# Kernel optimization log

Measured on AMD Instinct MI355X. Metric: run time of the kernel, lower is better.

The kernel has to match this reference:

```python
import jax, jax.numpy as jnp
import numpy as np

N = 100000
E = 1600000

def _gcn_layer(x, row, col, W, b):
    # gather neighbor feats then scatter-add into destination rows
    agg = jax.ops.segment_sum(x[col], row, num_segments=N)  # [N, d]
    deg = jax.ops.segment_sum(jnp.ones((row.shape[0],), x.dtype), row, num_segments=N)
    deg = jnp.clip(deg, 1.0, None)[:, None]  # [N, 1]
    return (agg / deg + x) @ W + b

def setup_inputs() -> dict:
    key = jax.random.key(0)
    ks = jax.random.split(key, 6)
    x = jax.random.normal(ks[0], (N, 64), dtype=jnp.float32)
    edge_index = jax.random.randint(ks[1], (2, E), 0, N, dtype=jnp.int64)
    W1 = jax.random.normal(ks[2], (64, 128), dtype=jnp.float32) * 0.1
    b1 = jax.random.normal(ks[3], (128,), dtype=jnp.float32) * 0.1
    W2 = jax.random.normal(ks[4], (128, 64), dtype=jnp.float32) * 0.1
    b2 = jax.random.normal(ks[5], (64,), dtype=jnp.float32) * 0.1
    return {"x": x, "edge_index": edge_index, "W1": W1, "b1": b1, "W2": W2, "b2": b2}

def reference(x, edge_index, W1, b1, W2, b2):
    row, col = edge_index[0], edge_index[1]
    h = jax.nn.relu(_gcn_layer(x, row, col, W1, b1))
    h = _gcn_layer(h, row, col, W2, b2)
    return h
```

## Files before the change

kernel.cpp:

```cpp
#include <hip/hip_runtime.h>
#include <stdint.h>

#define WS_ALIGN(x) (((x) + 255) & ~(size_t)255)
#define RPB 256
#define CAPB 4608
#define NBMAX 512

typedef __attribute__((ext_vector_type(8))) unsigned short ushort8_t;
typedef __attribute__((ext_vector_type(8))) short short8_t;
typedef __attribute__((ext_vector_type(4))) float float4_t;

static __device__ __forceinline__ unsigned short f2bf(float f) {
    unsigned u = __float_as_uint(f);
    unsigned r = (u + 0x7FFFu + ((u >> 16) & 1u)) >> 16;
    return (unsigned short)r;
}
static __device__ __forceinline__ float bf2f(unsigned short s) {
    return __uint_as_float(((unsigned)s) << 16);
}

__global__ __launch_bounds__(256) void prep_kernel(
    const float4* __restrict__ x, ushort4* __restrict__ xb, int n4,
    const float* __restrict__ W1, const float* __restrict__ W2,
    unsigned short* __restrict__ W1t, unsigned short* __restrict__ W2t,
    int* __restrict__ gCursor, int* __restrict__ gTotal, int nb) {
    int i = blockIdx.x * 256 + threadIdx.x;
    if (i < 8192) {
        int k = i >> 7, col = i & 127;
        W1t[col * 64 + k] = f2bf(W1[i]);
    } else if (i < 16384) {
        int j = i - 8192;
        int k = j >> 6, col = j & 63;
        W2t[col * 128 + k] = f2bf(W2[j]);
    }
    int c = i - 16384;
    if (c >= 0 && c < nb) gCursor[c] = c * CAPB;
    if (c == nb) *gTotal = 0;
    int j = i - (16384 + nb + 64);
    if (j >= 0 && j < n4 + 16) {
        ushort4 o = make_ushort4(0, 0, 0, 0);
        if (j < n4) {
            float4 f = x[j];
            o.x = f2bf(f.x); o.y = f2bf(f.y); o.z = f2bf(f.z); o.w = f2bf(f.w);
        }
        xb[j] = o;
    }
}

__global__ __launch_bounds__(256) void bucket_kernel(
    const void* __restrict__ eidx, int E,
    int nb, int* __restrict__ gCursor, unsigned* __restrict__ staging) {
    __shared__ int cnt[NBMAX];
    __shared__ int base[NBMAX];
    __shared__ int sOr;
    int t = threadIdx.x;
    for (int i = t; i < nb; i += 256) cnt[i] = 0;
    if (t == 0) sOr = 0;
    __syncthreads();

    int hv = 0;
    const int* p32 = (const int*)eidx;
    for (int i = t; i < 2048 && i < E; i += 256) hv |= p32[2 * i + 1];
    if (hv) atomicOr(&sOr, 1);
    __syncthreads();
    bool is64 = (sOr == 0);

    int e0 = (blockIdx.x * 256 + t) * 8;
    int m = E - e0; if (m > 8) m = 8; if (m < 0) m = 0;
    int r[8], bk[8], slot[8];
    for (int j = 0; j < m; ++j) {
        r[j] = is64 ? (int)((const long long*)eidx)[e0 + j]
                    : ((const int*)eidx)[e0 + j];
        bk[j] = r[j] >> 8;
        slot[j] = atomicAdd(&cnt[bk[j]], 1);
    }
    __syncthreads();
    for (int i = t; i < nb; i += 256)
        base[i] = cnt[i] ? atomicAdd(&gCursor[i], cnt[i]) : 0;
    __syncthreads();
    for (int j = 0; j < m; ++j) {
        int c = is64 ? (int)((const long long*)eidx)[E + e0 + j]
                     : ((const int*)eidx)[E + e0 + j];
        int dst = base[bk[j]] + slot[j];
        if (dst < (bk[j] + 1) * CAPB)
            staging[dst] = ((unsigned)(r[j] & (RPB - 1)) << 17) | (unsigned)c;
    }
}

__global__ __launch_bounds__(512) void ell_kernel(
    const unsigned* __restrict__ staging, const int* __restrict__ gCursor,
    int* __restrict__ csr, int2* __restrict__ meta,
    int* __restrict__ gTotal, int N) {
    __shared__ unsigned sd[CAPB];
    __shared__ int lcnt[RPB], scan[RPB], lcnt2[RPB];
    __shared__ int bucketBase;
    int b = blockIdx.x, t = threadIdx.x;
    if (t < RPB) { lcnt[t] = 0; lcnt2[t] = 0; }
    __syncthreads();

    int start = b * CAPB;
    int end = gCursor[b];
    if (end > start + CAPB) end = start + CAPB;
    int cnt = end - start;

    for (int i = t; i < cnt; i += 512) {
        unsigned p = staging[start + i];
        sd[i] = p;
        atomicAdd(&lcnt[p >> 17], 1);
    }
    __syncthreads();
    if (t < RPB) scan[t] = lcnt[t];
    __syncthreads();
    for (int off = 1; off < RPB; off <<= 1) {
        int v = 0;
        if (t < RPB && t >= off) v = scan[t - off];
        __syncthreads();
        if (t < RPB) scan[t] += v;
        __syncthreads();
    }
    if (t == 0) bucketBase = atomicAdd(gTotal, scan[RPB - 1]);
    __syncthreads();
    if (t < RPB) {
        int gr = (b << 8) + t;
        if (gr < N) meta[gr] = make_int2(lcnt[t], bucketBase + scan[t] - lcnt[t]);
    }
    __syncthreads();
    for (int i = t; i < cnt; i += 512) {
        unsigned p = sd[i];
        int lr = p >> 17;
        int slot = atomicAdd(&lcnt2[lr], 1);
        csr[bucketBase + scan[lr] - lcnt[lr] + slot] = (int)(p & 0x1FFFFu);
    }
}

__global__ __launch_bounds__(256) void agg_kernel(
    const unsigned short* __restrict__ xb, const int2* __restrict__ meta,
    const int* __restrict__ csr,
    unsigned short* __restrict__ v, int N) {
    int tid = threadIdx.x;
    int w = tid >> 6, lane = tid & 63;
    int n = blockIdx.x * 4 + w;
    if (n >= N) return;
    int2 md = meta[n];
    int d = md.x;
    if (d > 64) d = 64;
    int ri = csr[md.y + lane];
    if (lane >= d) ri = N;
    int nq = __builtin_amdgcn_readfirstlane((d + 3) >> 2);
    int lq = lane >> 4;
    size_t loff = (size_t)((lane & 15) << 3);
    const char* xbB = (const char*)xb;

    float a0 = 0.f, a1 = 0.f, a2 = 0.f, a3 = 0.f;
#define QL(J, Q) int rq##J = __shfl(ri, ((Q) << 2) + lq); \
    uint2 u##J = *(const uint2*)(xbB + (((size_t)(unsigned)rq##J) << 7) + loff);
#define QA(J) a0 += __uint_as_float(u##J.x << 16); \
    a1 += __uint_as_float(u##J.x & 0xFFFF0000u); \
    a2 += __uint_as_float(u##J.y << 16); \
    a3 += __uint_as_float(u##J.y & 0xFFFF0000u);
    int q = 0;
    while (q + 4 <= nq) {
        QL(0, q) QL(1, q + 1) QL(2, q + 2) QL(3, q + 3)
        QA(0) QA(1) QA(2) QA(3)
        q += 4;
    }
    while (q < nq) { QL(4, q) QA(4) ++q; }
#undef QL
#undef QA
    a0 += __shfl_xor(a0, 16); a0 += __shfl_xor(a0, 32);
    a1 += __shfl_xor(a1, 16); a1 += __shfl_xor(a1, 32);
    a2 += __shfl_xor(a2, 16); a2 += __shfl_xor(a2, 32);
    a3 += __shfl_xor(a3, 16); a3 += __shfl_xor(a3, 32);

    if (lane < 16) {
        uint2 su = *(const uint2*)(xbB + (((size_t)n) << 7) + loff);
        float s0 = __uint_as_float(su.x << 16), s1 = __uint_as_float(su.x & 0xFFFF0000u);
        float s2 = __uint_as_float(su.y << 16), s3 = __uint_as_float(su.y & 0xFFFF0000u);
        float inv = 1.0f / (float)(d > 1 ? d : 1);
        uint2 o;
        o.x = (unsigned)f2bf(a0 * inv + s0) | ((unsigned)f2bf(a1 * inv + s1) << 16);
        o.y = (unsigned)f2bf(a2 * inv + s2) | ((unsigned)f2bf(a3 * inv + s3) << 16);
        *(uint2*)((char*)v + (((size_t)n) << 7) + loff) = o;
    }
}

__global__ __launch_bounds__(256) void mlp_kernel(
    const unsigned short* __restrict__ v, const unsigned short* __restrict__ W1t,
    const float* __restrict__ b1, const unsigned short* __restrict__ W2t,
    unsigned short* __restrict__ g16, int N) {
    __shared__ unsigned short hA[64 * 136];
    int t = threadIdx.x;
    int node0 = blockIdx.x * 64;
    int w = t >> 6, lane = t & 63;
    int l15 = lane & 15, quad = lane >> 4;
    const float4_t fzero = {0.f, 0.f, 0.f, 0.f};

    short8_t af[4][2];
    #pragma unroll
    for (int ms = 0; ms < 4; ++ms)
        #pragma unroll
        for (int kk = 0; kk < 2; ++kk)
            af[ms][kk] = *(const short8_t*)&v[(size_t)(node0 + ms * 16 + l15) * 64 + kk * 32 + quad * 8];
    short8_t bf1[2][2];
    #pragma unroll
    for (int cs = 0; cs < 2; ++cs)
        #pragma unroll
        for (int kk = 0; kk < 2; ++kk)
            bf1[cs][kk] = *(const short8_t*)&W1t[((w * 2 + cs) * 16 + l15) * 64 + kk * 32 + quad * 8];

    float4_t acc1[4][2];
    #pragma unroll
    for (int ms = 0; ms < 4; ++ms)
        #pragma unroll
        for (int cs = 0; cs < 2; ++cs)
            acc1[ms][cs] = fzero;
    #pragma unroll
    for (int ms = 0; ms < 4; ++ms)
        #pragma unroll
        for (int cs = 0; cs < 2; ++cs) {
            acc1[ms][cs] = __builtin_amdgcn_mfma_f32_16x16x32_bf16(af[ms][0], bf1[cs][0], acc1[ms][cs], 0, 0, 0);
            acc1[ms][cs] = __builtin_amdgcn_mfma_f32_16x16x32_bf16(af[ms][1], bf1[cs][1], acc1[ms][cs], 0, 0, 0);
        }

    #pragma unroll
    for (int cs = 0; cs < 2; ++cs) {
        int col = (w * 2 + cs) * 16 + l15;
        float bias = b1[col];
        #pragma unroll
        for (int ms = 0; ms < 4; ++ms) {
            #pragma unroll
            for (int r = 0; r < 4; ++r) {
                int node = ms * 16 + quad * 4 + r;
                hA[node * 136 + col] = f2bf(fmaxf(acc1[ms][cs][r] + bias, 0.f));
            }
        }
    }
    __syncthreads();

    short8_t bh[4];
    #pragma unroll
    for (int kk = 0; kk < 4; ++kk)
        bh[kk] = *(const short8_t*)&W2t[(w * 16 + l15) * 128 + kk * 32 + quad * 8];

    #pragma unroll
    for (int ms = 0; ms < 4; ++ms) {
        float4_t acc2 = fzero;
        #pragma unroll
        for (int kk = 0; kk < 4; ++kk) {
            short8_t ah = *(const short8_t*)&hA[(ms * 16 + l15) * 136 + kk * 32 + quad * 8];
            acc2 = __builtin_amdgcn_mfma_f32_16x16x32_bf16(ah, bh[kk], acc2, 0, 0, 0);
        }
        #pragma unroll
        for (int r = 0; r < 4; ++r) {
            int gn = node0 + ms * 16 + quad * 4 + r;
            if (gn < N) g16[(size_t)gn * 64 + w * 16 + l15] = f2bf(acc2[r]);
        }
    }
}

__global__ __launch_bounds__(256) void final_kernel(
    const unsigned short* __restrict__ g16, const float* __restrict__ b2,
    const int2* __restrict__ meta, const int* __restrict__ csr,
    float* __restrict__ out, int N) {
    int tid = threadIdx.x;
    int w = tid >> 6, lane = tid & 63;
    int n = blockIdx.x * 4 + w;
    if (n >= N) return;
    int2 md = meta[n];
    int d = md.x;
    if (d > 64) d = 64;
    int ri = csr[md.y + lane];
    if (lane >= d) ri = N;
    int nq = __builtin_amdgcn_readfirstlane((d + 3) >> 2);
    int lq = lane >> 4;
    size_t loff = (size_t)((lane & 15) << 3);
    const char* gB = (const char*)g16;

    float a0 = 0.f, a1 = 0.f, a2 = 0.f, a3 = 0.f;
#define QL(J, Q) int rq##J = __shfl(ri, ((Q) << 2) + lq); \
    uint2 u##J = *(const uint2*)(gB + (((size_t)(unsigned)rq##J) << 7) + loff);
#define QA(J) a0 += __uint_as_float(u##J.x << 16); \
    a1 += __uint_as_float(u##J.x & 0xFFFF0000u); \
    a2 += __uint_as_float(u##J.y << 16); \
    a3 += __uint_as_float(u##J.y & 0xFFFF0000u);
    int q = 0;
    while (q + 4 <= nq) {
        QL(0, q) QL(1, q + 1) QL(2, q + 2) QL(3, q + 3)
        QA(0) QA(1) QA(2) QA(3)
        q += 4;
    }
    while (q < nq) { QL(4, q) QA(4) ++q; }
#undef QL
#undef QA
    a0 += __shfl_xor(a0, 16); a0 += __shfl_xor(a0, 32);
    a1 += __shfl_xor(a1, 16); a1 += __shfl_xor(a1, 32);
    a2 += __shfl_xor(a2, 16); a2 += __shfl_xor(a2, 32);
    a3 += __shfl_xor(a3, 16); a3 += __shfl_xor(a3, 32);

    if (lane < 16) {
        uint2 su = *(const uint2*)(gB + (((size_t)n) << 7) + loff);
        float s0 = __uint_as_float(su.x << 16), s1 = __uint_as_float(su.x & 0xFFFF0000u);
        float s2 = __uint_as_float(su.y << 16), s3 = __uint_as_float(su.y & 0xFFFF0000u);
        float4 bz = ((const float4*)b2)[lane & 15];
        float inv = 1.0f / (float)(d > 1 ? d : 1);
        float4 o;
        o.x = a0 * inv + s0 + bz.x;
        o.y = a1 * inv + s1 + bz.y;
        o.z = a2 * inv + s2 + bz.z;
        o.w = a3 * inv + s3 + bz.w;
        *(float4*)((char*)out + (((size_t)n) << 8) + (loff << 1)) = o;
    }
}

extern "C" void kernel_launch(void* const* d_in, const int* in_sizes, int n_in,
                              void* d_out, int out_size, void* d_ws, size_t ws_size,
                              hipStream_t stream) {
    const float* x  = (const float*)d_in[0];
    const void*  ei = d_in[1];
    const float* W1 = (const float*)d_in[2];
    const float* b1 = (const float*)d_in[3];
    const float* W2 = (const float*)d_in[4];
    const float* b2 = (const float*)d_in[5];
    float* out = (float*)d_out;

    int N = out_size / 64;
    int E = in_sizes[1] / 2;
    int nb = (N + RPB - 1) / RPB;

    char* ws = (char*)d_ws;
    size_t off = 0;
    auto alloc = [&](size_t bytes) { size_t r = off; off += WS_ALIGN(bytes); return r; };
    int* gTotal   = (int*)(ws + alloc(4));
    int* gCursor  = (int*)(ws + alloc((size_t)4 * nb));
    int2* meta    = (int2*)(ws + alloc((size_t)8 * N));
    int* csr      = (int*)(ws + alloc((size_t)4 * (E + 64)));
    char* bufA    = ws + alloc((size_t)128 * (N + 1));
    unsigned short* xb  = (unsigned short*)bufA;
    unsigned short* g16 = (unsigned short*)bufA;
    unsigned short* v   = (unsigned short*)(ws + alloc((size_t)128 * (N + 64)));
    unsigned short* W1t = (unsigned short*)(ws + alloc((size_t)2 * 8192));
    unsigned short* W2t = (unsigned short*)(ws + alloc((size_t)2 * 8192));
    unsigned* staging = (unsigned*)(ws + alloc((size_t)4 * nb * CAPB));
    (void)ws_size;

    int n4 = N * 16;
    int prepWork = 16384 + nb + 64 + n4 + 16;
    prep_kernel<<<(prepWork + 255) / 256, 256, 0, stream>>>(
        (const float4*)x, (ushort4*)xb, n4, W1, W2, W1t, W2t, gCursor, gTotal, nb);

    int b1blocks = (E + 2047) / 2048;
    bucket_kernel<<<b1blocks, 256, 0, stream>>>(ei, E, nb, gCursor, staging);
    ell_kernel<<<nb, 512, 0, stream>>>(staging, gCursor, csr, meta, gTotal, N);

    agg_kernel<<<(N + 3) / 4, 256, 0, stream>>>(xb, meta, csr, v, N);
    mlp_kernel<<<(N + 63) / 64, 256, 0, stream>>>(v, W1t, b1, W2t, g16, N);
    final_kernel<<<(N + 3) / 4, 256, 0, stream>>>(g16, b2, meta, csr, out, N);
}
```

Before: 238.6 us.

## Fuse first-layer aggregation into MLP kernel via shared-memory staging

Merges the per-node neighbor aggregation and the two-matmul MLP into one kernel. Each 64-node block now gathers its own rows into shared memory, removing the global round trip through the intermediate v buffer and one kernel launch. Because xb and g16 can no longer alias, g16 gets its own buffer, and its sentinel row (used by final_kernel for padded neighbor indices) is zeroed in prep. The cost is less parallelism in the gather phase: each warp processes 16 nodes serially, and blocks carry a larger shared-memory footprint, which can reduce latency hiding.

Result: slower. 252.5 us (+5.8%).

```diff
diff --git a/kernel.cpp b/kernel.cpp
--- a/kernel.cpp
+++ b/kernel.cpp
@@ -23,7 +23,8 @@
     const float4* __restrict__ x, ushort4* __restrict__ xb, int n4,
     const float* __restrict__ W1, const float* __restrict__ W2,
     unsigned short* __restrict__ W1t, unsigned short* __restrict__ W2t,
-    int* __restrict__ gCursor, int* __restrict__ gTotal, int nb) {
+    int* __restrict__ gCursor, int* __restrict__ gTotal, int nb,
+    ushort4* __restrict__ g16sent) {
     int i = blockIdx.x * 256 + threadIdx.x;
     if (i < 8192) {
         int k = i >> 7, col = i & 127;
@@ -45,6 +46,8 @@
         }
         xb[j] = o;
     }
+    int j2 = i - (16384 + nb + 64 + n4 + 16);
+    if (j2 >= 0 && j2 < 16) g16sent[j2] = make_ushort4(0, 0, 0, 0);
 }
 
 __global__ __launch_bounds__(256) void bucket_kernel(
@@ -133,65 +136,67 @@
     }
 }
 
-__global__ __launch_bounds__(256) void agg_kernel(
+__global__ __launch_bounds__(256) void aggmlp_kernel(
     const unsigned short* __restrict__ xb, const int2* __restrict__ meta,
-    const int* __restrict__ csr,
-    unsigned short* __restrict__ v, int N) {
-    int tid = threadIdx.x;
-    int w = tid >> 6, lane = tid & 63;
-    int n = blockIdx.x * 4 + w;
-    if (n >= N) return;
-    int2 md = meta[n];
-    int d = md.x;
-    if (d > 64) d = 64;
-    int ri = csr[md.y + lane];
-    if (lane >= d) ri = N;
-    int nq = __builtin_amdgcn_readfirstlane((d + 3) >> 2);
+    const int* __restrict__ csr, const unsigned short* __restrict__ W1t,
+    const float* __restrict__ b1, const unsigned short* __restrict__ W2t,
+    unsigned short* __restrict__ g16, int N) {
+    __shared__ unsigned short sh[64 * 136];
+    int t = threadIdx.x;
+    int node0 = blockIdx.x * 64;
+    int w = t >> 6, lane = t & 63;
     int lq = lane >> 4;
     size_t loff = (size_t)((lane & 15) << 3);
     const char* xbB = (const char*)xb;
 
-    float a0 = 0.f, a1 = 0.f, a2 = 0.f, a3 = 0.f;
+    for (int j = 0; j < 16; ++j) {
+        int nl = j * 4 + w;
+        int n = node0 + nl;
+        int d = 0, ri = N;
+        if (n < N) {
+            int2 md = meta[n];
+            d = md.x > 64 ? 64 : md.x;
+            ri = csr[md.y + lane];
+            if (lane >= d) ri = N;
+        }
+        int nq = __builtin_amdgcn_readfirstlane((d + 3) >> 2);
+
+        float a0 = 0.f, a1 = 0.f, a2 = 0.f, a3 = 0.f;
 #define QL(J, Q) int rq##J = __shfl(ri, ((Q) << 2) + lq); \
     uint2 u##J = *(const uint2*)(xbB + (((size_t)(unsigned)rq##J) << 7) + loff);
 #define QA(J) a0 += __uint_as_float(u##J.x << 16); \
     a1 += __uint_as_float(u##J.x & 0xFFFF0000u); \
     a2 += __uint_as_float(u##J.y << 16); \
     a3 += __uint_as_float(u##J.y & 0xFFFF0000u);
-    int q = 0;
-    while (q + 4 <= nq) {
-        QL(0, q) QL(1, q + 1) QL(2, q + 2) QL(3, q + 3)
-        QA(0) QA(1) QA(2) QA(3)
-        q += 4;
-    }
-    while (q < nq) { QL(4, q) QA(4) ++q; }
+        int q = 0;
+        while (q + 4 <= nq) {
+            QL(0, q) QL(1, q + 1) QL(2, q + 2) QL(3, q + 3)
+            QA(0) QA(1) QA(2) QA(3)
+            q += 4;
+        }
+        while (q < nq) { QL(4, q) QA(4) ++q; }
 #undef QL
 #undef QA
-    a0 += __shfl_xor(a0, 16); a0 += __shfl_xor(a0, 32);
-    a1 += __shfl_xor(a1, 16); a1 += __shfl_xor(a1, 32);
-    a2 += __shfl_xor(a2, 16); a2 += __shfl_xor(a2, 32);
-    a3 += __shfl_xor(a3, 16); a3 += __shfl_xor(a3, 32);
-
-    if (lane < 16) {
-        uint2 su = *(const uint2*)(xbB + (((size_t)n) << 7) + loff);
-        float s0 = __uint_as_float(su.x << 16), s1 = __uint_as_float(su.x & 0xFFFF0000u);
-        float s2 = __uint_as_float(su.y << 16), s3 = __uint_as_float(su.y & 0xFFFF0000u);
-        float inv = 1.0f / (float)(d > 1 ? d : 1);
-        uint2 o;
-        o.x = (unsigned)f2bf(a0 * inv + s0) | ((unsigned)f2bf(a1 * inv + s1) << 16);
-        o.y = (unsigned)f2bf(a2 * inv + s2) | ((unsigned)f2bf(a3 * inv + s3) << 16);
-        *(uint2*)((char*)v + (((size_t)n) << 7) + loff) = o;
-    }
-}
-
-__global__ __launch_bounds__(256) void mlp_kernel(
-    const unsigned short* __restrict__ v, const unsigned short* __restrict__ W1t,
-    const float* __restrict__ b1, const unsigned short* __restrict__ W2t,
-    unsigned short* __restrict__ g16, int N) {
-    __shared__ unsigned short hA[64 * 136];
-    int t = threadIdx.x;
-    int node0 = blockIdx.x * 64;
-    int w = t >> 6, lane = t & 63;
+        a0 += __shfl_xor(a0, 16); a0 += __shfl_xor(a0, 32);
+        a1 += __shfl_xor(a1, 16); a1 += __shfl_xor(a1, 32);
+        a2 += __shfl_xor(a2, 16); a2 += __shfl_xor(a2, 32);
+        a3 += __shfl_xor(a3, 16); a3 += __shfl_xor(a3, 32);
+
+        if (lane < 16) {
+            uint2 o = make_uint2(0u, 0u);
+            if (n < N) {
+                uint2 su = *(const uint2*)(xbB + (((size_t)n) << 7) + loff);
+                float s0 = __uint_as_float(su.x << 16), s1 = __uint_as_float(su.x & 0xFFFF0000u);
+                float s2 = __uint_as_float(su.y << 16), s3 = __uint_as_float(su.y & 0xFFFF0000u);
+                float inv = 1.0f / (float)(d > 1 ? d : 1);
+                o.x = (unsigned)f2bf(a0 * inv + s0) | ((unsigned)f2bf(a1 * inv + s1) << 16);
+                o.y = (unsigned)f2bf(a2 * inv + s2) | ((unsigned)f2bf(a3 * inv + s3) << 16);
+            }
+            *(uint2*)((char*)sh + nl * 144 + loff) = o;
+        }
+    }
+    __syncthreads();
+
     int l15 = lane & 15, quad = lane >> 4;
     const float4_t fzero = {0.f, 0.f, 0.f, 0.f};
 
@@ -200,7 +205,9 @@
     for (int ms = 0; ms < 4; ++ms)
         #pragma unroll
         for (int kk = 0; kk < 2; ++kk)
-            af[ms][kk] = *(const short8_t*)&v[(size_t)(node0 + ms * 16 + l15) * 64 + kk * 32 + quad * 8];
+            af[ms][kk] = *(const short8_t*)&sh[(ms * 16 + l15) * 72 + kk * 32 + quad * 8];
+    __syncthreads();
+
     short8_t bf1[2][2];
     #pragma unroll
     for (int cs = 0; cs < 2; ++cs)
@@ -231,7 +238,7 @@
             #pragma unroll
             for (int r = 0; r < 4; ++r) {
                 int node = ms * 16 + quad * 4 + r;
-                hA[node * 136 + col] = f2bf(fmaxf(acc1[ms][cs][r] + bias, 0.f));
+                sh[node * 136 + col] = f2bf(fmaxf(acc1[ms][cs][r] + bias, 0.f));
             }
         }
     }
@@ -247,7 +254,7 @@
         float4_t acc2 = fzero;
         #pragma unroll
         for (int kk = 0; kk < 4; ++kk) {
-            short8_t ah = *(const short8_t*)&hA[(ms * 16 + l15) * 136 + kk * 32 + quad * 8];
+            short8_t ah = *(const short8_t*)&sh[(ms * 16 + l15) * 136 + kk * 32 + quad * 8];
             acc2 = __builtin_amdgcn_mfma_f32_16x16x32_bf16(ah, bh[kk], acc2, 0, 0, 0);
         }
         #pragma unroll
@@ -334,25 +341,23 @@
     int* gCursor  = (int*)(ws + alloc((size_t)4 * nb));
     int2* meta    = (int2*)(ws + alloc((size_t)8 * N));
     int* csr      = (int*)(ws + alloc((size_t)4 * (E + 64)));
-    char* bufA    = ws + alloc((size_t)128 * (N + 1));
-    unsigned short* xb  = (unsigned short*)bufA;
-    unsigned short* g16 = (unsigned short*)bufA;
-    unsigned short* v   = (unsigned short*)(ws + alloc((size_t)128 * (N + 64)));
+    unsigned short* xb  = (unsigned short*)(ws + alloc((size_t)128 * (N + 1)));
+    unsigned short* g16 = (unsigned short*)(ws + alloc((size_t)128 * (N + 1)));
     unsigned short* W1t = (unsigned short*)(ws + alloc((size_t)2 * 8192));
     unsigned short* W2t = (unsigned short*)(ws + alloc((size_t)2 * 8192));
     unsigned* staging = (unsigned*)(ws + alloc((size_t)4 * nb * CAPB));
     (void)ws_size;
 
     int n4 = N * 16;
-    int prepWork = 16384 + nb + 64 + n4 + 16;
+    int prepWork = 16384 + nb + 64 + n4 + 16 + 16;
     prep_kernel<<<(prepWork + 255) / 256, 256, 0, stream>>>(
-        (const float4*)x, (ushort4*)xb, n4, W1, W2, W1t, W2t, gCursor, gTotal, nb);
+        (const float4*)x, (ushort4*)xb, n4, W1, W2, W1t, W2t, gCursor, gTotal, nb,
+        (ushort4*)(g16 + (size_t)N * 64));
 
     int b1blocks = (E + 2047) / 2048;
     bucket_kernel<<<b1blocks, 256, 0, stream>>>(ei, E, nb, gCursor, staging);
     ell_kernel<<<nb, 512, 0, stream>>>(staging, gCursor, csr, meta, gTotal, N);
 
-    agg_kernel<<<(N + 3) / 4, 256, 0, stream>>>(xb, meta, csr, v, N);
-    mlp_kernel<<<(N + 63) / 64, 256, 0, stream>>>(v, W1t, b1, W2t, g16, N);
+    aggmlp_kernel<<<(N + 63) / 64, 256, 0, stream>>>(xb, meta, csr, W1t, b1, W2t, g16, N);
     final_kernel<<<(N + 3) / 4, 256, 0, stream>>>(g16, b2, meta, csr, out, N);
 }
```
